# Performance work log

Hardware: AMD Instinct MI355X
Metric: run time of the kernel (lower is better)

## Reference

```python
import jax, jax.numpy as jnp
import numpy as np

D_IN, D_HEAD, D_EXPAND, D_OUT, H = 512, 64, 2048, 512, 8
D_Q = D_HEAD * H  # 512
D_K = D_HEAD * H  # 512
D_V = D_IN * H    # 4096 (non-standard: per-head value dim = d_in)
EPS = 1e-5


def layernorm(x, g, b):
    mu = jnp.mean(x, axis=-1, keepdims=True)
    var = jnp.mean(jnp.square(x - mu), axis=-1, keepdims=True)
    return (x - mu) * jax.lax.rsqrt(var + EPS) * g + b


def setup_inputs() -> dict:
    key = jax.random.key(0)
    ks = jax.random.split(key, 12)
    B, N = 2, 2048
    s_in = 1.0 / np.sqrt(D_IN)
    s_mh = 1.0 / np.sqrt(D_IN * H)
    s_ex = 1.0 / np.sqrt(D_EXPAND)
    return {
        "x": jax.random.normal(ks[0], (B, N, D_IN), jnp.float32),
        "ln1_g": jnp.ones((D_IN,), jnp.float32),
        "ln1_b": jnp.zeros((D_IN,), jnp.float32),
        "Wqkv": jax.random.normal(ks[1], (D_IN, D_Q + D_K + D_V), jnp.float32) * s_in,
        "bqkv": jax.random.normal(ks[2], (D_Q + D_K + D_V,), jnp.float32) * 0.01,
        "Wm": jax.random.normal(ks[3], (D_IN * H, D_IN), jnp.float32) * s_mh,
        "bm": jax.random.normal(ks[4], (D_IN,), jnp.float32) * 0.01,
        "ln2_g": jnp.ones((D_IN,), jnp.float32),
        "ln2_b": jnp.zeros((D_IN,), jnp.float32),
        "W1": jax.random.normal(ks[5], (D_IN, D_EXPAND), jnp.float32) * s_in,
        "b1": jax.random.normal(ks[6], (D_EXPAND,), jnp.float32) * 0.01,
        "W2": jax.random.normal(ks[7], (D_EXPAND, D_OUT), jnp.float32) * s_ex,
        "b2": jax.random.normal(ks[8], (D_OUT,), jnp.float32) * 0.01,
    }


def reference(x, ln1_g, ln1_b, Wqkv, bqkv, Wm, bm, ln2_g, ln2_b, W1, b1, W2, b2):
    B, N, _ = x.shape
    scale = D_HEAD ** -0.5
    qkv = layernorm(x, ln1_g, ln1_b) @ Wqkv + bqkv
    q, k, v = jnp.split(qkv, [D_Q, D_Q + D_K], axis=-1)
    q = q.reshape(B, N, H, D_HEAD).transpose(0, 2, 1, 3)  # (B,H,N,dh)
    k = k.reshape(B, N, H, D_HEAD).transpose(0, 2, 1, 3)
    v = v.reshape(B, N, H, D_IN).transpose(0, 2, 1, 3)    # (B,H,N,d_in)
    attn = jax.nn.softmax(jnp.einsum('bhnd,bhmd->bhnm', q, k) * scale, axis=-1)
    out = jnp.einsum('bhnm,bhmc->bhnc', attn, v)          # (B,H,N,d_in)
    out = out.transpose(0, 2, 1, 3).reshape(B, N, H * D_IN)
    x2 = x + out @ Wm + bm
    h = layernorm(x2, ln2_g, ln2_b) @ W1 + b1
    h = h * jax.nn.sigmoid(h)  # Swish
    return h @ W2 + b2 + x2    # shortcut = Identity (d_in == d_out)
```

## Files before the change

kernel.cpp:

```cpp
#include <hip/hip_runtime.h>
#include <cmath>

typedef unsigned short u16;
typedef unsigned int   u32;
typedef __attribute__((ext_vector_type(8))) __bf16 bf16x8;
typedef __attribute__((ext_vector_type(4))) float  f32x4;
typedef __attribute__((ext_vector_type(8))) unsigned short u16x8;
typedef __attribute__((ext_vector_type(4))) unsigned short u16x4;

#define DEV __device__ __forceinline__

DEV float bf2f(u16 u){ union{u32 i; float f;} v; v.i=((u32)u)<<16; return v.f; }
DEV u16 f2bf(float f){ union{float f; u32 i;} v; v.f=f; u32 r=v.i+0x7fffu+((v.i>>16)&1u); return (u16)(r>>16); }

#if defined(__has_builtin) && __has_builtin(__builtin_amdgcn_global_load_lds)
DEV void gld16(const void* g, void* l){
  __builtin_amdgcn_global_load_lds((__attribute__((address_space(1))) void*)g,
                                   (__attribute__((address_space(3))) void*)l, 16, 0, 0);
}
#else
DEV void gld16(const void* g, void* l){ *(u16x8*)l = *(const u16x8*)g; }
#endif

#if defined(__has_builtin) && __has_builtin(__builtin_amdgcn_exp2f)
DEV float fexp2(float x){ return __builtin_amdgcn_exp2f(x); }
#else
DEV float fexp2(float x){ return exp2f(x); }
#endif

DEV bool probe_f32(const u16* __restrict__ x)
{
  int sane = 0;
#pragma unroll
  for (int i = 0; i < 64; ++i){
    int e = (x[i] >> 7) & 0xFF;
    sane += (e >= 100 && e <= 150);
  }
  return sane < 56;
}

__global__ __launch_bounds__(256)
void conv_vecs(const void* a0,const void* a1,const void* a2,const void* a3,
               const void* a4,const void* a5,const void* a6,const void* a7,
               float* __restrict__ dst, const u16* __restrict__ xp,
               int* __restrict__ flagw)
{
  const bool f32 = probe_f32(xp);
  if (blockIdx.x==0 && threadIdx.x==0) *flagw = f32 ? 1 : 0;
  int i = blockIdx.x*256 + threadIdx.x;
  if (i >= 10240) return;
  const void* src; int off;
  if      (i < 512)  { src=a0; off=i; }
  else if (i < 1024) { src=a1; off=i-512; }
  else if (i < 6144) { src=a2; off=i-1024; }
  else if (i < 6656) { src=a3; off=i-6144; }
  else if (i < 7168) { src=a4; off=i-6656; }
  else if (i < 7680) { src=a5; off=i-7168; }
  else if (i < 9728) { src=a6; off=i-7680; }
  else               { src=a7; off=i-9728; }
  dst[i] = f32 ? ((const float*)src)[off] : bf2f(((const u16*)src)[off]);
}

#define SWZ_SRC(c) (((c)&7) ^ (((c)>>3)&7))

template<int SWZ>
DEV void remap_xcd(int& bx, int& by)
{
  if (SWZ==1){
    int L = by*(int)gridDim.x + bx;
    int xcd = L & 7, l = L >> 3;
    int chunk = (int)gridDim.x >> 3;
    bx = xcd*chunk + (l % chunk);
    by = l / chunk;
  } else if (SWZ==2){
    int L = by*(int)gridDim.x + bx;
    int xcd = L & 7, l = L >> 3;
    int chunk = (int)gridDim.y >> 3;
    by = xcd*chunk + (l % chunk);
    bx = l / chunk;
  }
}

template<int MODE, int SWZ, bool VT>
__global__ __launch_bounds__(512)
void gemm_bt(const u16* __restrict__ A, const u16* __restrict__ BT,
             void* __restrict__ C, const float* __restrict__ bias,
             int K, int lda, int ldb, int ldc, u16* __restrict__ vout)
{
  __shared__ u16 AB[4*128*64];
  u16* As0 = AB;
  u16* Bs0 = AB + 2*128*64;
  const int tid  = threadIdx.x;
  const int lane = tid & 63;
  const int quad = lane>>4, l7 = lane&7, l15 = lane&15;
  const int wv   = tid >> 6;
  const int wm   = wv >> 2, wn = wv & 3;
  int bx = blockIdx.x, by = blockIdx.y;
  remap_xcd<SWZ>(bx, by);
  const long m0 = (long)by * 128;
  const long n0 = (long)bx * 128;

  f32x4 acc[4][2];
#pragma unroll
  for (int i=0;i<4;i++)
#pragma unroll
    for (int j=0;j<2;j++) acc[i][j] = (f32x4){0.f,0.f,0.f,0.f};

  auto stage = [&](int bi, int k0){
#pragma unroll
    for (int i=0;i<2;i++){
      int c = i*512 + tid;
      gld16(A  + (m0 + (c>>3))*lda + k0 + SWZ_SRC(c)*8, &As0[bi*8192 + c*8]);
      gld16(BT + (n0 + (c>>3))*ldb + k0 + SWZ_SRC(c)*8, &Bs0[bi*8192 + c*8]);
    }
  };

  const int S = K >> 6;
  stage(0, 0);
  __syncthreads();

  for (int s=0; s<S; ++s){
    const int cb = s & 1;
    if (s+1 < S) stage(cb^1, (s+1)<<6);
#pragma unroll
    for (int kk=0;kk<2;kk++){
      const int ch = ((kk*4 + quad) ^ l7) * 8;
      bf16x8 af[4], bfr[2];
#pragma unroll
      for (int t=0;t<4;t++)
        af[t]  = *(const bf16x8*)&As0[cb*8192 + (wm*64 + t*16 + l15)*64 + ch];
#pragma unroll
      for (int t=0;t<2;t++)
        bfr[t] = *(const bf16x8*)&Bs0[cb*8192 + (wn*32 + t*16 + l15)*64 + ch];
#pragma unroll
      for (int ti=0;ti<4;ti++)
#pragma unroll
        for (int tj=0;tj<2;tj++)
          acc[ti][tj] = __builtin_amdgcn_mfma_f32_16x16x32_bf16(af[ti], bfr[tj], acc[ti][tj], 0,0,0);
    }
    __syncthreads();
  }

  if (VT && n0 >= 1024){
    const int hh   = (int)((n0 - 1024) >> 9);
    const int c0   = (int)((n0 - 1024) & 511);
    const int b_   = (int)(m0 >> 11);
    const int kloc = (int)(m0 & 2047);
    u16* vb = vout + ((long)(b_*8 + hh))*512*2048 + kloc;
    u16* Ts = AB;
#pragma unroll
    for (int ti=0;ti<4;ti++)
#pragma unroll
    for (int tj=0;tj<2;tj++)
#pragma unroll
    for (int r=0;r<4;r++){
      int row = wm*64 + ti*16 + quad*4 + r;
      int cl  = wn*32 + tj*16 + l15;
      Ts[row*132 + cl] = f2bf(acc[ti][tj][r] + bias[n0 + cl]);
    }
    __syncthreads();
#pragma unroll
    for (int step=0; step<4; ++step){
      int cr = step*32 + (tid>>4);
      int t8 = (tid&15)*8;
      u16x8 pk;
#pragma unroll
      for (int j=0;j<8;j++) pk[j] = Ts[(t8+j)*132 + cr];
      *(u16x8*)(vb + (long)(c0 + cr)*2048 + t8) = pk;
    }
    return;
  }

#pragma unroll
  for (int ti=0;ti<4;ti++)
#pragma unroll
  for (int tj=0;tj<2;tj++)
#pragma unroll
  for (int r=0;r<4;r++){
    long row = m0 + wm*64 + ti*16 + quad*4 + r;
    long col = n0 + wn*32 + tj*16 + l15;
    float v = acc[ti][tj][r] + bias[col];
    if (MODE==2) v = v / (1.f + __expf(-v));
    ((u16*)C)[row*ldc+col] = f2bf(v);
  }
}

template<int MODE, int SWZ>
__global__ __launch_bounds__(512)
void gemm_n64(const u16* __restrict__ A, const u16* __restrict__ BT,
              void* __restrict__ C, const float* __restrict__ bias,
              const void* __restrict__ res,
              int K, int lda, int ldb, int ldc, const int* __restrict__ flag)
{
  __shared__ u16 As[2][128*64];
  __shared__ u16 Bs[2][64*64];
  const int tid  = threadIdx.x;
  const int lane = tid & 63;
  const int quad = lane>>4, l7 = lane&7, l15 = lane&15;
  const int wm   = tid >> 6;
  int bx = blockIdx.x, by = blockIdx.y;
  remap_xcd<SWZ>(bx, by);
  const long m0 = (long)by * 128;
  const long n0 = (long)bx * 64;
  const bool f32io = flag && (*flag != 0);

  f32x4 acc[4];
#pragma unroll
  for (int j=0;j<4;j++) acc[j] = (f32x4){0.f,0.f,0.f,0.f};

  auto stage = [&](int bi, int k0){
#pragma unroll
    for (int i=0;i<2;i++){
      int c = i*512 + tid;
      gld16(A + (m0 + (c>>3))*lda + k0 + SWZ_SRC(c)*8, &As[bi][c*8]);
    }
    { int c = tid;
      gld16(BT + (n0 + (c>>3))*ldb + k0 + SWZ_SRC(c)*8, &Bs[bi][c*8]); }
  };

  const int S = K >> 6;
  stage(0, 0);
  __syncthreads();

  for (int s=0; s<S; ++s){
    const int cb = s & 1;
    if (s+1 < S) stage(cb^1, (s+1)<<6);
#pragma unroll
    for (int kk=0;kk<2;kk++){
      const int ch = ((kk*4 + quad) ^ l7) * 8;
      bf16x8 af = *(const bf16x8*)&As[cb][(wm*16 + l15)*64 + ch];
      bf16x8 bfr[4];
#pragma unroll
      for (int t=0;t<4;t++)
        bfr[t] = *(const bf16x8*)&Bs[cb][(t*16 + l15)*64 + ch];
#pragma unroll
      for (int tj=0;tj<4;tj++)
        acc[tj] = __builtin_amdgcn_mfma_f32_16x16x32_bf16(af, bfr[tj], acc[tj], 0,0,0);
    }
    __syncthreads();
  }

#pragma unroll
  for (int tj=0;tj<4;tj++)
#pragma unroll
  for (int r=0;r<4;r++){
    long row = m0 + wm*16 + quad*4 + r;
    long col = n0 + tj*16 + l15;
    float v = acc[tj][r] + bias[col];
    if (MODE==1){
      v += f32io ? ((const float*)res)[row*ldc+col]
                 : bf2f(((const u16*)res)[row*ldc+col]);
      ((float*)C)[row*ldc+col] = v;
    } else {
      v += ((const float*)res)[row*ldc+col];
      if (f32io) ((float*)C)[row*ldc+col] = v;
      else       ((u16*)C)[row*ldc+col]   = f2bf(v);
    }
  }
}

__global__ __launch_bounds__(512, 2)
void att_flash(const u16* __restrict__ qkv, const u16* __restrict__ vt,
               u16* __restrict__ ao)
{
  __shared__ u16 Qs[128*64];
  __shared__ u16 Ks[2][64*64];
  __shared__ u16 Ps[128*68];
  __shared__ u16 Vs[512*64];
  __shared__ float alph[8];
  __shared__ float l_lds[128];
  __shared__ int resc[2];
  const int tid=threadIdx.x, lane=tid&63, wv=tid>>6;
  const int wm=wv>>2, wn=wv&3;
  const int quad=lane>>4, l7=lane&7, l15=lane&15;
  const int bid = blockIdx.x;
  const int id  = ((bid&7)<<5) + (bid>>3);
  const int qt  = id & 15, bh = id >> 4;
  const int b = bh>>3, h = bh&7;
  const long q0 = (long)qt*128;
  const u16* qb = qkv + ((long)b*2048 + q0)*5120 + h*64;
  const u16* kb = qkv + (long)b*2048*5120 + 512 + h*64;
  const u16* vb = vt + (long)bh*512*2048;

#pragma unroll
  for (int i=0;i<2;i++){
    int c=i*512+tid;
    gld16(qb + (long)(c>>3)*5120 + SWZ_SRC(c)*8, &Qs[c*8]);
  }
  { int c=tid; gld16(kb + (long)(c>>3)*5120 + SWZ_SRC(c)*8, &Ks[0][c*8]); }
  if (tid==0){ resc[0]=0; resc[1]=0; }

  union { u16x8 u; bf16x8 v; } one_u;
#pragma unroll
  for (int j=0;j<8;j++) one_u.u[j] = 0x3F80;
  const bf16x8 ones = one_u.v;

  f32x4 o[4][8];
#pragma unroll
  for (int i=0;i<4;i++)
#pragma unroll
    for (int j=0;j<8;j++) o[i][j] = (f32x4){0.f,0.f,0.f,0.f};
  f32x4 ol[4];
#pragma unroll
  for (int i=0;i<4;i++) ol[i] = (f32x4){0.f,0.f,0.f,0.f};
  float m_w = -1e30f;

  __syncthreads();
  bf16x8 qreg[2];
#pragma unroll
  for (int kk=0;kk<2;kk++)
    qreg[kk] = *(const bf16x8*)&Qs[(wv*16 + l15)*64 + ((kk*4 + quad) ^ l7)*8];

  for (int mt=0; mt<32; ++mt){
    const long m0 = (long)mt*64;
    const int cur = mt&1;
    __syncthreads();

    if (mt < 31){ int c=tid; gld16(kb + (m0+64 + (c>>3))*5120 + SWZ_SRC(c)*8, &Ks[cur^1][c*8]); }
#pragma unroll
    for (int i=0;i<8;i++){
      int c=i*512+tid;
      gld16(vb + (long)(c>>3)*2048 + m0 + SWZ_SRC(c)*8, &Vs[c*8]);
    }
    if (tid==0) resc[cur^1] = 0;

    f32x4 s[4];
#pragma unroll
    for (int j=0;j<4;j++) s[j] = (f32x4){0.f,0.f,0.f,0.f};
#pragma unroll
    for (int kk=0;kk<2;kk++){
      const int ch = ((kk*4 + quad) ^ l7) * 8;
#pragma unroll
      for (int tj=0;tj<4;tj++){
        bf16x8 bfr = *(const bf16x8*)&Ks[cur][(tj*16 + l15)*64 + ch];
        s[tj] = __builtin_amdgcn_mfma_f32_16x16x32_bf16(qreg[kk], bfr, s[tj], 0,0,0);
      }
    }

    float vm = s[0][0];
#pragma unroll
    for (int tj=0;tj<4;tj++)
#pragma unroll
      for (int r=0;r<4;r++) vm = fmaxf(vm, s[tj][r]);
    vm = fmaxf(vm, __shfl_xor(vm,1));  vm = fmaxf(vm, __shfl_xor(vm,2));
    vm = fmaxf(vm, __shfl_xor(vm,4));  vm = fmaxf(vm, __shfl_xor(vm,8));
    vm = fmaxf(vm, __shfl_xor(vm,16)); vm = fmaxf(vm, __shfl_xor(vm,32));
    const float vs = vm*0.125f;
    const bool c_ = (vs > m_w + 8.f);
    const float nm = c_ ? vs : m_w;
    const float al = c_ ? __expf(m_w - nm) : 1.f;
    m_w = nm;
    const float nml = nm*1.44269504f;
#pragma unroll
    for (int tj=0;tj<4;tj++)
#pragma unroll
    for (int r=0;r<4;r++){
      float pv = fexp2(fmaf(s[tj][r], 0.18033688f, -nml));
      Ps[(wv*16 + quad*4 + r)*68 + tj*16 + l15] = f2bf(pv);
    }
    if (lane==0){ alph[wv] = al; if (c_) resc[cur] = 1; }
    __syncthreads();

    if (resc[cur]){
      float a_[4];
#pragma unroll
      for (int ti=0;ti<4;ti++) a_[ti] = alph[wm*4 + ti];
#pragma unroll
      for (int ti=0;ti<4;ti++)
#pragma unroll
      for (int tj=0;tj<8;tj++)
#pragma unroll
        for (int r=0;r<4;r++) o[ti][tj][r] *= a_[ti];
      if (wn==0){
#pragma unroll
        for (int ti=0;ti<4;ti++)
#pragma unroll
          for (int r=0;r<4;r++) ol[ti][r] *= a_[ti];
      }
    }
#pragma unroll
    for (int kk=0;kk<2;kk++){
      const int ch = ((kk*4 + quad) ^ l7) * 8;
      bf16x8 af[4], bfr[8];
#pragma unroll
      for (int t=0;t<4;t++){
        int base = (wm*64 + t*16 + l15)*68 + kk*32 + quad*8;
        union { u16x4 hh[2]; bf16x8 v; } u;
        u.hh[0] = *(const u16x4*)&Ps[base];
        u.hh[1] = *(const u16x4*)&Ps[base+4];
        af[t] = u.v;
      }
#pragma unroll
      for (int t=0;t<8;t++)
        bfr[t] = *(const bf16x8*)&Vs[(wn*128 + t*16 + l15)*64 + ch];
#pragma unroll
      for (int ti=0;ti<4;ti++)
#pragma unroll
        for (int tj=0;tj<8;tj++)
          o[ti][tj] = __builtin_amdgcn_mfma_f32_16x16x32_bf16(af[ti], bfr[tj], o[ti][tj], 0,0,0);
      if (wn==0){
#pragma unroll
        for (int ti=0;ti<4;ti++)
          ol[ti] = __builtin_amdgcn_mfma_f32_16x16x32_bf16(af[ti], ones, ol[ti], 0,0,0);
      }
    }
  }

  if (wn==0 && l15==0){
#pragma unroll
    for (int ti=0;ti<4;ti++)
#pragma unroll
      for (int r=0;r<4;r++) l_lds[wm*64 + ti*16 + quad*4 + r] = ol[ti][r];
  }
  __syncthreads();
  float rl[4][4];
#pragma unroll
  for (int ti=0;ti<4;ti++)
#pragma unroll
    for (int r=0;r<4;r++) rl[ti][r] = 1.f / l_lds[wm*64 + ti*16 + quad*4 + r];
#pragma unroll
  for (int ti=0;ti<4;ti++)
#pragma unroll
  for (int tj=0;tj<8;tj++)
#pragma unroll
  for (int r=0;r<4;r++){
    long rown = q0 + wm*64 + ti*16 + quad*4 + r;
    long col  = wn*128 + tj*16 + l15;
    ao[((long)b*2048 + rown)*4096 + (long)h*512 + col] = f2bf(o[ti][tj][r]*rl[ti][r]);
  }
}

template<int SRC>
__global__ __launch_bounds__(256)
void ln_kernel(const void* __restrict__ xin, const float* __restrict__ g,
               const float* __restrict__ bb, u16* __restrict__ out,
               const int* __restrict__ flag)
{
  const int tid=threadIdx.x, lane=tid&63, wv=tid>>6;
  const long row = (long)blockIdx.x*4 + wv;
  const bool f32 = (SRC==1) || (flag && *flag != 0);
  float v[8];
  if (f32){
    const float* xr = (const float*)xin + row*512 + lane*8;
#pragma unroll
    for (int j=0;j<8;j++) v[j]=xr[j];
  } else {
    const u16* xr = (const u16*)xin + row*512 + lane*8;
    u16x8 xv = *(const u16x8*)xr;
#pragma unroll
    for (int j=0;j<8;j++) v[j]=bf2f(xv[j]);
  }
  float s1=0.f, s2=0.f;
#pragma unroll
  for (int j=0;j<8;j++){ s1+=v[j]; s2+=v[j]*v[j]; }
  for (int off=1; off<64; off<<=1){ s1+=__shfl_xor(s1,off); s2+=__shfl_xor(s2,off); }
  float mu  = s1*(1.f/512.f);
  float var = s2*(1.f/512.f) - mu*mu;
  float rs  = rsqrtf(var + 1e-5f);
  u16x8 ov;
#pragma unroll
  for (int j=0;j<8;j++){
    int col = lane*8+j;
    ov[j] = f2bf((v[j]-mu)*rs*g[col] + bb[col]);
  }
  *(u16x8*)(out + row*512 + lane*8) = ov;
}

__global__ __launch_bounds__(256)
void transpose_all(const void* __restrict__ i0, const void* __restrict__ i1,
                   const void* __restrict__ i2, const void* __restrict__ i3,
                   u16* __restrict__ o0, u16* __restrict__ o1,
                   u16* __restrict__ o2, u16* __restrict__ o3,
                   const int* __restrict__ flag)
{
  __shared__ u16 t[32][33];
  const int bt = blockIdx.x;
  const void* in_; u16* out; int ldi, ldo, txn, lt;
  if (bt < 2560)      { in_=i0; out=o0; ldi=5120; ldo=512;  txn=160; lt=bt; }
  else if (bt < 4608) { in_=i1; out=o1; ldi=512;  ldo=4096; txn=16;  lt=bt-2560; }
  else if (bt < 5632) { in_=i2; out=o2; ldi=2048; ldo=512;  txn=64;  lt=bt-4608; }
  else                { in_=i3; out=o3; ldi=512;  ldo=2048; txn=16;  lt=bt-5632; }
  const int bx = lt % txn, by = lt / txn;
  const bool f32 = *flag != 0;
  const int tx = threadIdx.x, ty = threadIdx.y;
  const long c  = (long)bx*32 + tx;
  const long r0 = (long)by*32;
  if (f32){
    const float* in = (const float*)in_;
#pragma unroll
    for (int j=0;j<4;j++) t[ty+j*8][tx] = f2bf(in[(r0+ty+j*8)*ldi + c]);
  } else {
    const u16* in = (const u16*)in_;
#pragma unroll
    for (int j=0;j<4;j++) t[ty+j*8][tx] = in[(r0+ty+j*8)*ldi + c];
  }
  __syncthreads();
  const long rr = r0 + tx;
  const long cc = (long)bx*32 + ty;
#pragma unroll
  for (int j=0;j<4;j++) out[(cc+j*8)*ldo + rr] = t[tx][ty+j*8];
}

extern "C" void kernel_launch(void* const* d_in, const int* in_sizes, int n_in,
                              void* d_out, int out_size, void* d_ws, size_t ws_size,
                              hipStream_t stream)
{
  const void* x    = d_in[0];
  const void* ln1g = d_in[1];
  const void* ln1b = d_in[2];
  const void* Wqkv = d_in[3];
  const void* bqkv = d_in[4];
  const void* Wm   = d_in[5];
  const void* bm   = d_in[6];
  const void* ln2g = d_in[7];
  const void* ln2b = d_in[8];
  const void* W1   = d_in[9];
  const void* b1   = d_in[10];
  const void* W2   = d_in[11];
  const void* b2   = d_in[12];

  char* p = (char*)d_ws;
  auto take = [&](size_t n){ void* r=(void*)p; p += (n + 255) & ~(size_t)255; return r; };
  u16*   lnb   = (u16*)  take((size_t)4096*512*2);
  u16*   qkv   = (u16*)  take((size_t)4096*5120*2);
  u16*   vtb   = (u16*)  take((size_t)16*512*2048*2);
  u16*   wqkvT = (u16*)  take((size_t)5120*512*2);
  u16*   wmT   = (u16*)  take((size_t)512*4096*2);
  u16*   w1T   = (u16*)  take((size_t)2048*512*2);
  u16*   w2T   = (u16*)  take((size_t)512*2048*2);
  u16*   ao    = (u16*)  take((size_t)4096*4096*2);
  float* cvec  = (float*)take((size_t)10240*4);
  int*   flag  = (int*)  take(4);
  float* x2    = (float*)vtb;
  u16*   hb    = qkv;

  conv_vecs<<<40, 256, 0, stream>>>(ln1g, ln1b, bqkv, bm, ln2g, ln2b, b1, b2,
                                    cvec, (const u16*)x, flag);

  transpose_all<<<6656, dim3(32,8), 0, stream>>>(Wqkv, Wm, W1, W2,
                                                 wqkvT, wmT, w1T, w2T, flag);

  ln_kernel<0><<<1024, 256, 0, stream>>>(x, cvec+0, cvec+512, lnb, flag);
  gemm_bt<0,1,true><<<dim3(40,32), 512, 0, stream>>>(lnb, wqkvT, qkv, cvec+1024,
                                                     512, 512, 512, 5120, vtb);

  att_flash<<<dim3(256), 512, 0, stream>>>(qkv, vtb, ao);

  gemm_n64<1,2><<<dim3(8,32), 512, 0, stream>>>(ao, wmT, x2, cvec+6144, x,
                                                4096, 4096, 4096, 512, flag);
  ln_kernel<1><<<1024, 256, 0, stream>>>(x2, cvec+6656, cvec+7168, lnb, nullptr);
  gemm_bt<2,2,false><<<dim3(16,32), 512, 0, stream>>>(lnb, w1T, hb, cvec+7680,
                                                      512, 512, 512, 2048, nullptr);
  gemm_n64<3,2><<<dim3(8,32), 512, 0, stream>>>(hb, w2T, d_out, cvec+9728, x2,
                                                2048, 2048, 2048, 512, flag);
}
```

Baseline: 356.1 us.

## Shrink attention tiles to 64 query rows and 32-key blocks for higher occupancy

```diff
diff --git a/kernel.cpp b/kernel.cpp
--- a/kernel.cpp
+++ b/kernel.cpp
@@ -259,35 +259,34 @@
   }
 }
 
-__global__ __launch_bounds__(512, 2)
+__global__ __launch_bounds__(512, 4)
 void att_flash(const u16* __restrict__ qkv, const u16* __restrict__ vt,
                u16* __restrict__ ao)
 {
-  __shared__ u16 Qs[128*64];
-  __shared__ u16 Ks[2][64*64];
-  __shared__ u16 Ps[128*68];
-  __shared__ u16 Vs[512*64];
-  __shared__ float alph[8];
-  __shared__ float l_lds[128];
+  __shared__ u16 Ks[2][32*64];
+  __shared__ u16 Ps[64*36];
+  __shared__ u16 Vs[512*32];
+  __shared__ float alph[4];
+  __shared__ float l_lds[64];
   __shared__ int resc[2];
   const int tid=threadIdx.x, lane=tid&63, wv=tid>>6;
-  const int wm=wv>>2, wn=wv&3;
   const int quad=lane>>4, l7=lane&7, l15=lane&15;
   const int bid = blockIdx.x;
-  const int id  = ((bid&7)<<5) + (bid>>3);
-  const int qt  = id & 15, bh = id >> 4;
+  const int id  = ((bid&7)<<6) + (bid>>3);
+  const int qt  = id & 31, bh = id >> 5;
   const int b = bh>>3, h = bh&7;
-  const long q0 = (long)qt*128;
+  const long q0 = (long)qt*64;
   const u16* qb = qkv + ((long)b*2048 + q0)*5120 + h*64;
   const u16* kb = qkv + (long)b*2048*5120 + 512 + h*64;
   const u16* vb = vt + (long)bh*512*2048;
 
-#pragma unroll
-  for (int i=0;i<2;i++){
-    int c=i*512+tid;
-    gld16(qb + (long)(c>>3)*5120 + SWZ_SRC(c)*8, &Qs[c*8]);
-  }
-  { int c=tid; gld16(kb + (long)(c>>3)*5120 + SWZ_SRC(c)*8, &Ks[0][c*8]); }
+  bf16x8 qreg[2];
+  if (wv < 4){
+#pragma unroll
+    for (int kk=0;kk<2;kk++)
+      qreg[kk] = *(const bf16x8*)(qb + (long)(wv*16 + l15)*5120 + (kk*4+quad)*8);
+  }
+  if (tid < 256){ int c=tid; gld16(kb + (long)(c>>3)*5120 + SWZ_SRC(c)*8, &Ks[0][c*8]); }
   if (tid==0){ resc[0]=0; resc[1]=0; }
 
   union { u16x8 u; bf16x8 v; } one_u;
@@ -295,137 +294,135 @@
   for (int j=0;j<8;j++) one_u.u[j] = 0x3F80;
   const bf16x8 ones = one_u.v;
 
-  f32x4 o[4][8];
+  f32x4 o[4][4];
 #pragma unroll
   for (int i=0;i<4;i++)
 #pragma unroll
-    for (int j=0;j<8;j++) o[i][j] = (f32x4){0.f,0.f,0.f,0.f};
+    for (int j=0;j<4;j++) o[i][j] = (f32x4){0.f,0.f,0.f,0.f};
   f32x4 ol[4];
 #pragma unroll
   for (int i=0;i<4;i++) ol[i] = (f32x4){0.f,0.f,0.f,0.f};
   float m_w = -1e30f;
 
   __syncthreads();
-  bf16x8 qreg[2];
-#pragma unroll
-  for (int kk=0;kk<2;kk++)
-    qreg[kk] = *(const bf16x8*)&Qs[(wv*16 + l15)*64 + ((kk*4 + quad) ^ l7)*8];
-
-  for (int mt=0; mt<32; ++mt){
-    const long m0 = (long)mt*64;
+
+  for (int mt=0; mt<64; ++mt){
     const int cur = mt&1;
-    __syncthreads();
-
-    if (mt < 31){ int c=tid; gld16(kb + (m0+64 + (c>>3))*5120 + SWZ_SRC(c)*8, &Ks[cur^1][c*8]); }
-#pragma unroll
-    for (int i=0;i<8;i++){
-      int c=i*512+tid;
-      gld16(vb + (long)(c>>3)*2048 + m0 + SWZ_SRC(c)*8, &Vs[c*8]);
+    const long m0 = (long)mt*32;
+
+#pragma unroll
+    for (int i=0;i<4;i++){
+      int c = i*512 + tid;
+      int row = c>>2, k4 = c&3;
+      gld16(vb + (long)row*2048 + m0 + ((k4 ^ (row&3)))*8, &Vs[c*8]);
+    }
+    if (mt < 63 && tid < 256){
+      int c = tid;
+      gld16(kb + (m0+32 + (c>>3))*5120 + SWZ_SRC(c)*8, &Ks[cur^1][c*8]);
     }
     if (tid==0) resc[cur^1] = 0;
 
-    f32x4 s[4];
-#pragma unroll
-    for (int j=0;j<4;j++) s[j] = (f32x4){0.f,0.f,0.f,0.f};
-#pragma unroll
-    for (int kk=0;kk<2;kk++){
-      const int ch = ((kk*4 + quad) ^ l7) * 8;
-#pragma unroll
-      for (int tj=0;tj<4;tj++){
-        bf16x8 bfr = *(const bf16x8*)&Ks[cur][(tj*16 + l15)*64 + ch];
-        s[tj] = __builtin_amdgcn_mfma_f32_16x16x32_bf16(qreg[kk], bfr, s[tj], 0,0,0);
+    if (wv < 4){
+      f32x4 s[2];
+      s[0] = (f32x4){0.f,0.f,0.f,0.f}; s[1] = (f32x4){0.f,0.f,0.f,0.f};
+#pragma unroll
+      for (int kk=0;kk<2;kk++){
+        const int ch = ((kk*4 + quad) ^ l7) * 8;
+#pragma unroll
+        for (int tj=0;tj<2;tj++){
+          bf16x8 bfr = *(const bf16x8*)&Ks[cur][(tj*16 + l15)*64 + ch];
+          s[tj] = __builtin_amdgcn_mfma_f32_16x16x32_bf16(qreg[kk], bfr, s[tj], 0,0,0);
+        }
       }
-    }
-
-    float vm = s[0][0];
-#pragma unroll
-    for (int tj=0;tj<4;tj++)
-#pragma unroll
-      for (int r=0;r<4;r++) vm = fmaxf(vm, s[tj][r]);
-    vm = fmaxf(vm, __shfl_xor(vm,1));  vm = fmaxf(vm, __shfl_xor(vm,2));
-    vm = fmaxf(vm, __shfl_xor(vm,4));  vm = fmaxf(vm, __shfl_xor(vm,8));
-    vm = fmaxf(vm, __shfl_xor(vm,16)); vm = fmaxf(vm, __shfl_xor(vm,32));
-    const float vs = vm*0.125f;
-    const bool c_ = (vs > m_w + 8.f);
-    const float nm = c_ ? vs : m_w;
-    const float al = c_ ? __expf(m_w - nm) : 1.f;
-    m_w = nm;
-    const float nml = nm*1.44269504f;
-#pragma unroll
-    for (int tj=0;tj<4;tj++)
-#pragma unroll
-    for (int r=0;r<4;r++){
-      float pv = fexp2(fmaf(s[tj][r], 0.18033688f, -nml));
-      Ps[(wv*16 + quad*4 + r)*68 + tj*16 + l15] = f2bf(pv);
-    }
-    if (lane==0){ alph[wv] = al; if (c_) resc[cur] = 1; }
+      float vm = fmaxf(fmaxf(fmaxf(s[0][0],s[0][1]),fmaxf(s[0][2],s[0][3])),
+                       fmaxf(fmaxf(s[1][0],s[1][1]),fmaxf(s[1][2],s[1][3])));
+      vm = fmaxf(vm, __shfl_xor(vm,1));  vm = fmaxf(vm, __shfl_xor(vm,2));
+      vm = fmaxf(vm, __shfl_xor(vm,4));  vm = fmaxf(vm, __shfl_xor(vm,8));
+      vm = fmaxf(vm, __shfl_xor(vm,16)); vm = fmaxf(vm, __shfl_xor(vm,32));
+      const float vs = vm*0.125f;
+      const bool c_ = (vs > m_w + 8.f);
+      const float nm = c_ ? vs : m_w;
+      const float al = c_ ? __expf(m_w - nm) : 1.f;
+      m_w = nm;
+      const float nml = nm*1.44269504f;
+#pragma unroll
+      for (int tj=0;tj<2;tj++)
+#pragma unroll
+      for (int r=0;r<4;r++){
+        float pv = fexp2(fmaf(s[tj][r], 0.18033688f, -nml));
+        Ps[(wv*16 + quad*4 + r)*36 + tj*16 + l15] = f2bf(pv);
+      }
+      if (lane==0){ alph[wv] = al; if (c_) resc[cur] = 1; }
+    }
     __syncthreads();
 
     if (resc[cur]){
       float a_[4];
 #pragma unroll
-      for (int ti=0;ti<4;ti++) a_[ti] = alph[wm*4 + ti];
+      for (int ti=0;ti<4;ti++) a_[ti] = alph[ti];
 #pragma unroll
       for (int ti=0;ti<4;ti++)
 #pragma unroll
-      for (int tj=0;tj<8;tj++)
+      for (int tj=0;tj<4;tj++)
 #pragma unroll
         for (int r=0;r<4;r++) o[ti][tj][r] *= a_[ti];
-      if (wn==0){
+      if (wv==0){
 #pragma unroll
         for (int ti=0;ti<4;ti++)
 #pragma unroll
           for (int r=0;r<4;r++) ol[ti][r] *= a_[ti];
       }
     }
-#pragma unroll
-    for (int kk=0;kk<2;kk++){
-      const int ch = ((kk*4 + quad) ^ l7) * 8;
-      bf16x8 af[4], bfr[8];
+    {
+      bf16x8 af[4], bfr[4];
 #pragma unroll
       for (int t=0;t<4;t++){
-        int base = (wm*64 + t*16 + l15)*68 + kk*32 + quad*8;
+        int base = (t*16 + l15)*36 + quad*8;
         union { u16x4 hh[2]; bf16x8 v; } u;
         u.hh[0] = *(const u16x4*)&Ps[base];
         u.hh[1] = *(const u16x4*)&Ps[base+4];
         af[t] = u.v;
       }
 #pragma unroll
-      for (int t=0;t<8;t++)
-        bfr[t] = *(const bf16x8*)&Vs[(wn*128 + t*16 + l15)*64 + ch];
+      for (int t=0;t<4;t++){
+        int cr = wv*64 + t*16 + l15;
+        int p  = (quad ^ (cr&3)) * 8;
+        bfr[t] = *(const bf16x8*)&Vs[cr*32 + p];
+      }
 #pragma unroll
       for (int ti=0;ti<4;ti++)
 #pragma unroll
-        for (int tj=0;tj<8;tj++)
+        for (int tj=0;tj<4;tj++)
           o[ti][tj] = __builtin_amdgcn_mfma_f32_16x16x32_bf16(af[ti], bfr[tj], o[ti][tj], 0,0,0);
-      if (wn==0){
+      if (wv==0){
 #pragma unroll
         for (int ti=0;ti<4;ti++)
           ol[ti] = __builtin_amdgcn_mfma_f32_16x16x32_bf16(af[ti], ones, ol[ti], 0,0,0);
       }
     }
-  }
-
-  if (wn==0 && l15==0){
+    __syncthreads();
+  }
+
+  if (wv==0 && l15==0){
 #pragma unroll
     for (int ti=0;ti<4;ti++)
 #pragma unroll
-      for (int r=0;r<4;r++) l_lds[wm*64 + ti*16 + quad*4 + r] = ol[ti][r];
+      for (int r=0;r<4;r++) l_lds[ti*16 + quad*4 + r] = ol[ti][r];
   }
   __syncthreads();
   float rl[4][4];
 #pragma unroll
   for (int ti=0;ti<4;ti++)
 #pragma unroll
-    for (int r=0;r<4;r++) rl[ti][r] = 1.f / l_lds[wm*64 + ti*16 + quad*4 + r];
+    for (int r=0;r<4;r++) rl[ti][r] = 1.f / l_lds[ti*16 + quad*4 + r];
 #pragma unroll
   for (int ti=0;ti<4;ti++)
 #pragma unroll
-  for (int tj=0;tj<8;tj++)
+  for (int tj=0;tj<4;tj++)
 #pragma unroll
   for (int r=0;r<4;r++){
-    long rown = q0 + wm*64 + ti*16 + quad*4 + r;
-    long col  = wn*128 + tj*16 + l15;
+    long rown = q0 + ti*16 + quad*4 + r;
+    long col  = wv*64 + tj*16 + l15;
     ao[((long)b*2048 + rown)*4096 + (long)h*512 + col] = f2bf(o[ti][tj][r]*rl[ti][r]);
   }
 }
@@ -544,7 +541,7 @@
   gemm_bt<0,1,true><<<dim3(40,32), 512, 0, stream>>>(lnb, wqkvT, qkv, cvec+1024,
                                                      512, 512, 512, 5120, vtb);
 
-  att_flash<<<dim3(256), 512, 0, stream>>>(qkv, vtb, ao);
+  att_flash<<<dim3(512), 512, 0, stream>>>(qkv, vtb, ao);
 
   gemm_n64<1,2><<<dim3(8,32), 512, 0, stream>>>(ao, wmT, x2, cvec+6144, x,
                                                 4096, 4096, 4096, 512, flag);
```

New measurement: 435.0 us. +22.1%, slower.
